# Performance work log

Hardware: AMD Instinct MI355X
Metric: run time of the kernel (lower is better)

## Reference

```python
import jax, jax.numpy as jnp
import numpy as np

NUM_GROUPS = 32
EPS = 1e-5


def group_norm(x, scale, bias):
    # x: [b, c, h, w]
    b, c, h, w = x.shape
    xg = x.reshape(b, NUM_GROUPS, c // NUM_GROUPS, h, w)
    mean = jnp.mean(xg, axis=(2, 3, 4), keepdims=True)
    var = jnp.var(xg, axis=(2, 3, 4), keepdims=True)
    xg = (xg - mean) * jax.lax.rsqrt(var + EPS)
    xn = xg.reshape(b, c, h, w)
    return xn * scale[None, :, None, None] + bias[None, :, None, None]


def conv1x1(x, w, b):
    # x: [b, c_in, h, w], w: [c_out, c_in], b: [c_out]
    return jnp.einsum('bchw,dc->bdhw', x, w) + b[None, :, None, None]


def setup_inputs() -> dict:
    key = jax.random.key(0)
    ks = jax.random.split(key, 11)
    B, C, H, W = 16, 512, 32, 32
    s = 1.0 / np.sqrt(C)
    inp = {
        'x': jax.random.normal(ks[0], (B, C, H, W), jnp.float32),
        'gn_scale': jnp.ones((C,), jnp.float32),
        'gn_bias': jnp.zeros((C,), jnp.float32),
        'wq': jax.random.normal(ks[1], (C, C), jnp.float32) * s,
        'bq': jnp.zeros((C,), jnp.float32),
        'wk': jax.random.normal(ks[2], (C, C), jnp.float32) * s,
        'bk': jnp.zeros((C,), jnp.float32),
        'wv': jax.random.normal(ks[3], (C, C), jnp.float32) * s,
        'bv': jnp.zeros((C,), jnp.float32),
        'wp': jax.random.normal(ks[4], (C, C), jnp.float32) * s,
        'bp': jnp.zeros((C,), jnp.float32),
    }
    return inp


def reference(x, gn_scale, gn_bias, wq, bq, wk, bk, wv, bv, wp, bp):
    b, c, h, w = x.shape
    xn = group_norm(x, gn_scale, gn_bias)
    q = conv1x1(xn, wq, bq).reshape(b, c, h * w)  # [b, c, n]
    k = conv1x1(xn, wk, bk).reshape(b, c, h * w)
    v = conv1x1(xn, wv, bv).reshape(b, c, h * w)
    # attn[b, i, j] = sum_c q[b, c, i] * k[b, c, j]
    attn = jnp.einsum('bci,bcj->bij', q, k) * (c ** -0.5)
    A = jax.nn.softmax(attn, axis=-1)
    # out[b, c, i] = sum_j A[b, i, j] * v[b, c, j]
    out = jnp.einsum('bij,bcj->bci', A, v).reshape(b, c, h, w)
    scores = conv1x1(out, wp, bp)
    return x + scores
```

## Files before the change

### kernel.cpp

```cpp
#include <hip/hip_runtime.h>

typedef __bf16 bf16x8 __attribute__((ext_vector_type(8)));
typedef float  f32x4  __attribute__((ext_vector_type(4)));

__device__ __forceinline__ unsigned short f2bf(float f) {
    union { float f; unsigned int u; } x; x.f = f;
    unsigned int r = (x.u + 0x7FFFu + ((x.u >> 16) & 1u)) >> 16;
    return (unsigned short)r;
}
__device__ __forceinline__ float bf2f(unsigned int hi) {
    union { unsigned int u; float f; } x; x.u = hi; return x.f;
}

typedef const __attribute__((address_space(1))) unsigned short gu16;
typedef __attribute__((address_space(3)))       unsigned short lu16;
__device__ __forceinline__ void gl_lds16(const unsigned short* g, unsigned short* l) {
    __builtin_amdgcn_global_load_lds((gu16*)g, (lu16*)l, 16, 0, 0);
}

__device__ __forceinline__ void stage_tiles(
    const unsigned short* __restrict__ Ab, int lda,
    const unsigned short* __restrict__ Bb, int ldb,
    int k0, unsigned short* Ad, unsigned short* Bd,
    int wave, int r0, int c0)
{
    gl_lds16(Ab + (long)r0 * lda + c0 + k0,        Ad + wave * 512);
    gl_lds16(Ab + (long)(r0 + 64) * lda + c0 + k0, Ad + 2048 + wave * 512);
    gl_lds16(Bb + (long)r0 * ldb + c0 + k0,        Bd + wave * 512);
    gl_lds16(Bb + (long)(r0 + 64) * ldb + c0 + k0, Bd + 2048 + wave * 512);
}

__device__ __forceinline__ void gemm_core_db(
    const unsigned short* __restrict__ Ab, int lda,
    const unsigned short* __restrict__ Bb, int ldb,
    int K, f32x4 (&acc)[4][4],
    unsigned short* As, unsigned short* Bs)
{
    const int tid  = threadIdx.x;
    const int lane = tid & 63;
    const int wave = tid >> 6;
    const int wm   = (wave >> 1) * 64;
    const int wn   = (wave & 1) * 64;
    const int l16  = lane & 15;
    const int quad = lane >> 4;

    const int r0 = wave * 16 + (lane >> 2);
    const int c0 = (lane & 3) * 8;

    stage_tiles(Ab, lda, Bb, ldb, 0, As, Bs, wave, r0, c0);

    int sel = 0;
    for (int k0 = 0; k0 < K; k0 += 32) {
        __syncthreads();
        if (k0 + 32 < K)
            stage_tiles(Ab, lda, Bb, ldb, k0 + 32,
                        As + (sel ^ 1) * 4096, Bs + (sel ^ 1) * 4096, wave, r0, c0);

        const unsigned short* Ap = As + sel * 4096;
        const unsigned short* Bp = Bs + sel * 4096;
        bf16x8 af[4], bfr[4];
        #pragma unroll
        for (int mi = 0; mi < 4; mi++)
            af[mi] = *(const bf16x8*)&Ap[(wm + mi * 16 + l16) * 32 + quad * 8];
        #pragma unroll
        for (int ni = 0; ni < 4; ni++)
            bfr[ni] = *(const bf16x8*)&Bp[(wn + ni * 16 + l16) * 32 + quad * 8];
        #pragma unroll
        for (int mi = 0; mi < 4; mi++)
            #pragma unroll
            for (int ni = 0; ni < 4; ni++)
                acc[mi][ni] = __builtin_amdgcn_mfma_f32_16x16x32_bf16(af[mi], bfr[ni], acc[mi][ni], 0, 0, 0);
        sel ^= 1;
    }
}

template<typename OutT, bool TRANS_OUT, bool HAS_BIAS, bool HAS_RESID,
         bool EXP_SUM, bool ROW_SCALE>
__global__ __launch_bounds__(256) void gemm_k(
    const unsigned short* __restrict__ Ag, long sA, int lda,
    const unsigned short* __restrict__ Bg, long sB, int ldb,
    OutT* __restrict__ Cg, long sC, int ldc,
    const float* __restrict__ bias,
    const float* __restrict__ resid, long sR,
    float* __restrict__ lsum, long sL,
    float alpha, int K)
{
    __shared__ __align__(16) unsigned short As[2 * 4096];
    __shared__ __align__(16) unsigned short Bs[2 * 4096];

    const unsigned short* Ab = Ag + (long)blockIdx.z * sA + (long)(blockIdx.y * 128) * lda;
    const unsigned short* Bb = Bg + (long)blockIdx.z * sB + (long)(blockIdx.x * 128) * ldb;

    f32x4 acc[4][4] = {};
    gemm_core_db(Ab, lda, Bb, ldb, K, acc, As, Bs);

    const int lane = threadIdx.x & 63;
    const int wave = threadIdx.x >> 6;
    const int l16  = lane & 15;
    const int quad = lane >> 4;
    const int mb = blockIdx.y * 128 + (wave >> 1) * 64;
    const int nb = blockIdx.x * 128 + (wave & 1) * 64;

    #pragma unroll
    for (int mi = 0; mi < 4; mi++) {
        float rsum[4];
        if constexpr (EXP_SUM) { rsum[0] = rsum[1] = rsum[2] = rsum[3] = 0.f; }
        #pragma unroll
        for (int ni = 0; ni < 4; ni++) {
            f32x4 v = acc[mi][ni];
            const int m0 = mb + mi * 16 + quad * 4;
            const int n  = nb + ni * 16 + l16;
            float o[4];
            float invl;
            if constexpr (ROW_SCALE) invl = 1.f / lsum[(long)blockIdx.z * sL + n];
            #pragma unroll
            for (int r = 0; r < 4; r++) {
                float val = v[r] * alpha;
                if (HAS_BIAS) val += bias[m0 + r];
                if constexpr (EXP_SUM) { val = __expf(val); rsum[r] += val; }
                if constexpr (ROW_SCALE) val *= invl;
                o[r] = val;
            }
            if constexpr (!TRANS_OUT) {
                const long base = (long)blockIdx.z * sC;
                #pragma unroll
                for (int r = 0; r < 4; r++) {
                    float val = o[r];
                    if (HAS_RESID) val += resid[(long)blockIdx.z * sR + (long)(m0 + r) * ldc + n];
                    long idx = base + (long)(m0 + r) * ldc + n;
                    if constexpr (sizeof(OutT) == 2) ((unsigned short*)Cg)[idx] = f2bf(val);
                    else                              ((float*)Cg)[idx] = val;
                }
            } else {
                const long idx = (long)blockIdx.z * sC + (long)n * ldc + m0;
                if constexpr (sizeof(OutT) == 2) {
                    ushort4 p; p.x = f2bf(o[0]); p.y = f2bf(o[1]); p.z = f2bf(o[2]); p.w = f2bf(o[3]);
                    *(ushort4*)((unsigned short*)Cg + idx) = p;
                } else {
                    float4 p; p.x = o[0]; p.y = o[1]; p.z = o[2]; p.w = o[3];
                    *(float4*)((float*)Cg + idx) = p;
                }
            }
        }
        if constexpr (EXP_SUM) {
            const int m0 = mb + mi * 16 + quad * 4;
            #pragma unroll
            for (int r = 0; r < 4; r++) {
                float s = rsum[r];
                s += __shfl_xor(s, 1); s += __shfl_xor(s, 2);
                s += __shfl_xor(s, 4); s += __shfl_xor(s, 8);
                if (l16 == 0)
                    atomicAdd(&lsum[(long)blockIdx.z * sL + m0 + r], s);
            }
        }
    }
}

__global__ __launch_bounds__(256) void qkv_k(
    const unsigned short* __restrict__ Wqkv,
    const unsigned short* __restrict__ xnT,
    unsigned short* __restrict__ qT,
    unsigned short* __restrict__ kT,
    unsigned short* __restrict__ vB,
    const float* __restrict__ bqkv)
{
    __shared__ __align__(16) unsigned short As[2 * 4096];
    __shared__ __align__(16) unsigned short Bs[2 * 4096];

    const unsigned short* Ab = Wqkv + (long)(blockIdx.y * 128) * 512;
    const unsigned short* Bb = xnT + (long)blockIdx.z * 524288 + (long)(blockIdx.x * 128) * 512;

    f32x4 acc[4][4] = {};
    gemm_core_db(Ab, 512, Bb, 512, 512, acc, As, Bs);

    const int lane = threadIdx.x & 63;
    const int wave = threadIdx.x >> 6;
    const int l16  = lane & 15;
    const int quad = lane >> 4;
    const int mb = blockIdx.y * 128 + (wave >> 1) * 64;
    const int nb = blockIdx.x * 128 + (wave & 1) * 64;

    const int mat = blockIdx.y >> 2;
    const long zb = (long)blockIdx.z * 524288;

    #pragma unroll
    for (int mi = 0; mi < 4; mi++) {
        #pragma unroll
        for (int ni = 0; ni < 4; ni++) {
            f32x4 v = acc[mi][ni];
            const int m0 = mb + mi * 16 + quad * 4;
            const int n  = nb + ni * 16 + l16;
            float o[4];
            #pragma unroll
            for (int r = 0; r < 4; r++) o[r] = v[r] + bqkv[m0 + r];
            const int ml = m0 & 511;
            if (mat == 2) {
                #pragma unroll
                for (int r = 0; r < 4; r++)
                    vB[zb + (long)(ml + r) * 1024 + n] = f2bf(o[r]);
            } else {
                unsigned short* dst = (mat == 0) ? qT : kT;
                ushort4 p; p.x = f2bf(o[0]); p.y = f2bf(o[1]); p.z = f2bf(o[2]); p.w = f2bf(o[3]);
                *(ushort4*)(dst + zb + (long)n * 512 + ml) = p;
            }
        }
    }
}

__global__ __launch_bounds__(256) void gn_k(
    const float* __restrict__ x, const float* __restrict__ gsc,
    const float* __restrict__ gbi, unsigned short* __restrict__ xnT)
{
    __shared__ __align__(16) unsigned short ln[16 * 1024];
    __shared__ float red[8];
    const int b = blockIdx.y, g = blockIdx.x;
    const int tid = threadIdx.x, lane = tid & 63, wv = tid >> 6;

    const float4* x4 = (const float4*)(x + ((long)b * 512 + g * 16) * 1024);
    float4 vals[16];
    float s = 0.f, ss = 0.f;
    #pragma unroll
    for (int i = 0; i < 16; i++) {
        float4 v = x4[tid + i * 256];
        vals[i] = v;
        s  += v.x + v.y + v.z + v.w;
        ss += v.x * v.x + v.y * v.y + v.z * v.z + v.w * v.w;
    }
    for (int o = 32; o; o >>= 1) { s += __shfl_down(s, o); ss += __shfl_down(ss, o); }
    if (lane == 0) { red[wv * 2] = s; red[wv * 2 + 1] = ss; }
    __syncthreads();
    const float S  = red[0] + red[2] + red[4] + red[6];
    const float SS = red[1] + red[3] + red[5] + red[7];
    const float mean = S * (1.f / 16384.f);
    const float var  = SS * (1.f / 16384.f) - mean * mean;
    const float inv  = rsqrtf(var + 1e-5f);

    #pragma unroll
    for (int i = 0; i < 16; i++) {
        const int idx = tid + i * 256;
        const int c   = idx >> 8;
        const float sc = gsc[g * 16 + c] * inv;
        const float bi = gbi[g * 16 + c] - mean * sc;
        float4 v = vals[i];
        ushort4 p;
        p.x = f2bf(v.x * sc + bi); p.y = f2bf(v.y * sc + bi);
        p.z = f2bf(v.z * sc + bi); p.w = f2bf(v.w * sc + bi);
        ((ushort4*)ln)[idx] = p;
    }
    __syncthreads();

    unsigned short* op = xnT + (long)b * 1024 * 512 + g * 16;
    for (int rep = 0; rep < 4; rep++) {
        const int n = rep * 256 + tid;
        union { unsigned short u[16]; uint4 v[2]; } t;
        #pragma unroll
        for (int c = 0; c < 16; c++) t.u[c] = ln[c * 1024 + n];
        *(uint4*)&op[(long)n * 512]     = t.v[0];
        *(uint4*)&op[(long)n * 512 + 8] = t.v[1];
    }
}

__global__ __launch_bounds__(256) void wconv_k(
    const float* __restrict__ w0, const float* __restrict__ w1,
    const float* __restrict__ w2, const float* __restrict__ w3,
    const float* __restrict__ b0, const float* __restrict__ b1,
    const float* __restrict__ b2,
    unsigned short* __restrict__ out, float* __restrict__ bqkv,
    float* __restrict__ lsum)
{
    const int m = blockIdx.y;
    const int i = blockIdx.x * 256 + threadIdx.x;
    if (m == 4) {
        if (i < 384) {
            const int which = i >> 7, off = i & 127;
            const float* src = (which == 0) ? b0 : (which == 1) ? b1 : b2;
            ((float4*)bqkv)[i] = ((const float4*)src)[off];
        }
        if (i < 16384) lsum[i] = 0.f;
        return;
    }
    const float* src = (m == 0) ? w0 : (m == 1) ? w1 : (m == 2) ? w2 : w3;
    float4 v = ((const float4*)src)[i];
    ushort4 o; o.x = f2bf(v.x); o.y = f2bf(v.y); o.z = f2bf(v.z); o.w = f2bf(v.w);
    ((ushort4*)(out + (long)m * 262144))[i] = o;
}

extern "C" void kernel_launch(void* const* d_in, const int* in_sizes, int n_in,
                              void* d_out, int out_size, void* d_ws, size_t ws_size,
                              hipStream_t stream)
{
    const float* x   = (const float*)d_in[0];
    const float* gsc = (const float*)d_in[1];
    const float* gbi = (const float*)d_in[2];
    const float* wq  = (const float*)d_in[3];
    const float* bq  = (const float*)d_in[4];
    const float* wk  = (const float*)d_in[5];
    const float* bk  = (const float*)d_in[6];
    const float* wv  = (const float*)d_in[7];
    const float* bv  = (const float*)d_in[8];
    const float* wp  = (const float*)d_in[9];
    const float* bp  = (const float*)d_in[10];
    float* out = (float*)d_out;

    char* ws = (char*)d_ws;
    unsigned short* xnT = (unsigned short*)(ws);
    unsigned short* qT  = (unsigned short*)(ws + 16777216);
    unsigned short* kT  = (unsigned short*)(ws + 33554432);
    unsigned short* vB  = (unsigned short*)(ws + 50331648);
    unsigned short* Sb  = (unsigned short*)(ws + 67108864);
    unsigned short* Wb  = (unsigned short*)(ws + 100663296);
    float*          bqkv= (float*)        (ws + 102760448);
    float*          Lb  = (float*)        (ws + 102768640);
    unsigned short* OT  = xnT;

    const long sBCN = 512L * 1024;

    wconv_k<<<dim3(256, 5), 256, 0, stream>>>(wq, wk, wv, wp, bq, bk, bv, Wb, bqkv, Lb);
    gn_k<<<dim3(32, 16), 256, 0, stream>>>(x, gsc, gbi, xnT);

    qkv_k<<<dim3(8, 12, 16), 256, 0, stream>>>(Wb, xnT, qT, kT, vB, bqkv);

    gemm_k<unsigned short, false, false, false, true, false>
        <<<dim3(8, 8, 16), 256, 0, stream>>>(
        qT, sBCN, 512, kT, sBCN, 512, Sb, 1048576L, 1024, nullptr, nullptr, 0,
        Lb, 1024, 0.044194173824159216f, 512);

    gemm_k<unsigned short, true, false, false, false, true>
        <<<dim3(8, 4, 16), 256, 0, stream>>>(
        vB, sBCN, 1024, Sb, 1048576L, 1024, OT, sBCN, 512,
        nullptr, nullptr, 0, Lb, 1024, 1.f, 1024);

    gemm_k<float, false, true, true, false, false>
        <<<dim3(8, 4, 16), 256, 0, stream>>>(
        Wb + 786432, 0, 512, OT, sBCN, 512, out, sBCN, 1024, bp, x, sBCN,
        nullptr, 0, 1.f, 512);
}
```

Baseline: 239.4 us.

## Swizzle LDS GEMM tiles and stage bf16 epilogue through LDS for 16-byte stores

Applies an XOR swizzle to the 16-byte column chunks of the A/B tiles, on both the global-to-LDS staging side and the MFMA fragment read side, to reduce LDS bank conflicts. The bf16-output epilogues of the generic GEMM and the QKV kernel now write each wave's 64x64 tile into a swizzled LDS scratch area, then read it back and emit coalesced 16-byte global stores, replacing scattered 2-byte or 8-byte stores. This adds two barriers and some LDS traffic per block and reuses the operand buffers as scratch.

```diff
diff --git a/kernel.cpp b/kernel.cpp
--- a/kernel.cpp
+++ b/kernel.cpp
@@ -7,9 +7,6 @@
     union { float f; unsigned int u; } x; x.f = f;
     unsigned int r = (x.u + 0x7FFFu + ((x.u >> 16) & 1u)) >> 16;
     return (unsigned short)r;
-}
-__device__ __forceinline__ float bf2f(unsigned int hi) {
-    union { unsigned int u; float f; } x; x.u = hi; return x.f;
 }
 
 typedef const __attribute__((address_space(1))) unsigned short gu16;
@@ -45,9 +42,11 @@
     const int quad = lane >> 4;
 
     const int r0 = wave * 16 + (lane >> 2);
-    const int c0 = (lane & 3) * 8;
+    const int c0 = ((lane & 3) ^ ((lane >> 3) & 3)) * 8;
 
     stage_tiles(Ab, lda, Bb, ldb, 0, As, Bs, wave, r0, c0);
+
+    const int sw8 = ((l16 >> 1) & 3) * 8;
 
     int sel = 0;
     for (int k0 = 0; k0 < K; k0 += 32) {
@@ -61,10 +60,10 @@
         bf16x8 af[4], bfr[4];
         #pragma unroll
         for (int mi = 0; mi < 4; mi++)
-            af[mi] = *(const bf16x8*)&Ap[(wm + mi * 16 + l16) * 32 + quad * 8];
+            af[mi] = *(const bf16x8*)&Ap[(wm + mi * 16 + l16) * 32 + ((quad * 8) ^ sw8)];
         #pragma unroll
         for (int ni = 0; ni < 4; ni++)
-            bfr[ni] = *(const bf16x8*)&Bp[(wn + ni * 16 + l16) * 32 + quad * 8];
+            bfr[ni] = *(const bf16x8*)&Bp[(wn + ni * 16 + l16) * 32 + ((quad * 8) ^ sw8)];
         #pragma unroll
         for (int mi = 0; mi < 4; mi++)
             #pragma unroll
@@ -85,8 +84,9 @@
     float* __restrict__ lsum, long sL,
     float alpha, int K)
 {
-    __shared__ __align__(16) unsigned short As[2 * 4096];
-    __shared__ __align__(16) unsigned short Bs[2 * 4096];
+    __shared__ __align__(16) unsigned short LB[16384];
+    unsigned short* As = LB;
+    unsigned short* Bs = LB + 8192;
 
     const unsigned short* Ab = Ag + (long)blockIdx.z * sA + (long)(blockIdx.y * 128) * lda;
     const unsigned short* Bb = Bg + (long)blockIdx.z * sB + (long)(blockIdx.x * 128) * ldb;
@@ -101,56 +101,92 @@
     const int mb = blockIdx.y * 128 + (wave >> 1) * 64;
     const int nb = blockIdx.x * 128 + (wave & 1) * 64;
 
-    #pragma unroll
-    for (int mi = 0; mi < 4; mi++) {
-        float rsum[4];
-        if constexpr (EXP_SUM) { rsum[0] = rsum[1] = rsum[2] = rsum[3] = 0.f; }
-        #pragma unroll
-        for (int ni = 0; ni < 4; ni++) {
-            f32x4 v = acc[mi][ni];
-            const int m0 = mb + mi * 16 + quad * 4;
-            const int n  = nb + ni * 16 + l16;
-            float o[4];
-            float invl;
-            if constexpr (ROW_SCALE) invl = 1.f / lsum[(long)blockIdx.z * sL + n];
-            #pragma unroll
-            for (int r = 0; r < 4; r++) {
-                float val = v[r] * alpha;
-                if (HAS_BIAS) val += bias[m0 + r];
-                if constexpr (EXP_SUM) { val = __expf(val); rsum[r] += val; }
-                if constexpr (ROW_SCALE) val *= invl;
-                o[r] = val;
-            }
-            if constexpr (!TRANS_OUT) {
+    if constexpr (sizeof(OutT) == 2) {
+        __syncthreads();
+        unsigned short* scr = LB + wave * 4096;
+
+        #pragma unroll
+        for (int mi = 0; mi < 4; mi++) {
+            float rsum[4];
+            if constexpr (EXP_SUM) { rsum[0] = rsum[1] = rsum[2] = rsum[3] = 0.f; }
+            #pragma unroll
+            for (int ni = 0; ni < 4; ni++) {
+                f32x4 v = acc[mi][ni];
+                float invl;
+                if constexpr (ROW_SCALE) invl = 1.f / lsum[(long)blockIdx.z * sL + nb + ni * 16 + l16];
+                float o[4];
+                #pragma unroll
+                for (int r = 0; r < 4; r++) {
+                    float val = v[r] * alpha;
+                    if constexpr (HAS_BIAS) val += bias[mb + mi * 16 + quad * 4 + r];
+                    if constexpr (EXP_SUM) { val = __expf(val); rsum[r] += val; }
+                    if constexpr (ROW_SCALE) val *= invl;
+                    o[r] = val;
+                }
+                if constexpr (TRANS_OUT) {
+                    const int nl = ni * 16 + l16;
+                    const int ch = mi * 2 + (quad >> 1);
+                    ushort4 p; p.x = f2bf(o[0]); p.y = f2bf(o[1]); p.z = f2bf(o[2]); p.w = f2bf(o[3]);
+                    *(ushort4*)&scr[nl * 64 + ((ch ^ (nl & 7)) * 8) + (quad & 1) * 4] = p;
+                } else {
+                    #pragma unroll
+                    for (int r = 0; r < 4; r++) {
+                        const int ml = mi * 16 + quad * 4 + r;
+                        const int nc = ni * 2 + (l16 >> 3);
+                        scr[ml * 64 + ((nc ^ (ml & 7)) * 8) + (l16 & 7)] = f2bf(o[r]);
+                    }
+                }
+            }
+            if constexpr (EXP_SUM) {
+                const int m0 = mb + mi * 16 + quad * 4;
+                #pragma unroll
+                for (int r = 0; r < 4; r++) {
+                    float s = rsum[r];
+                    s += __shfl_xor(s, 1); s += __shfl_xor(s, 2);
+                    s += __shfl_xor(s, 4); s += __shfl_xor(s, 8);
+                    if (l16 == 0)
+                        atomicAdd(&lsum[(long)blockIdx.z * sL + m0 + r], s);
+                }
+            }
+        }
+        __syncthreads();
+
+        const int ch2 = lane & 7;
+        const int rr  = lane >> 3;
+        unsigned short* Cs = (unsigned short*)Cg + (long)blockIdx.z * sC;
+        if constexpr (TRANS_OUT) {
+            unsigned short* dst = Cs + mb + ch2 * 8;
+            #pragma unroll
+            for (int it = 0; it < 8; it++) {
+                const int nl = rr + it * 8;
+                uint4 v = *(uint4*)&scr[nl * 64 + ((ch2 ^ (nl & 7)) * 8)];
+                *(uint4*)(dst + (long)(nb + nl) * ldc) = v;
+            }
+        } else {
+            unsigned short* dst = Cs + nb + ch2 * 8;
+            #pragma unroll
+            for (int it = 0; it < 8; it++) {
+                const int ml = rr + it * 8;
+                uint4 v = *(uint4*)&scr[ml * 64 + ((ch2 ^ (ml & 7)) * 8)];
+                *(uint4*)(dst + (long)(mb + ml) * ldc) = v;
+            }
+        }
+    } else {
+        #pragma unroll
+        for (int mi = 0; mi < 4; mi++) {
+            #pragma unroll
+            for (int ni = 0; ni < 4; ni++) {
+                f32x4 v = acc[mi][ni];
+                const int m0 = mb + mi * 16 + quad * 4;
+                const int n  = nb + ni * 16 + l16;
                 const long base = (long)blockIdx.z * sC;
                 #pragma unroll
                 for (int r = 0; r < 4; r++) {
-                    float val = o[r];
+                    float val = v[r] * alpha;
+                    if (HAS_BIAS) val += bias[m0 + r];
                     if (HAS_RESID) val += resid[(long)blockIdx.z * sR + (long)(m0 + r) * ldc + n];
-                    long idx = base + (long)(m0 + r) * ldc + n;
-                    if constexpr (sizeof(OutT) == 2) ((unsigned short*)Cg)[idx] = f2bf(val);
-                    else                              ((float*)Cg)[idx] = val;
+                    ((float*)Cg)[base + (long)(m0 + r) * ldc + n] = val;
                 }
-            } else {
-                const long idx = (long)blockIdx.z * sC + (long)n * ldc + m0;
-                if constexpr (sizeof(OutT) == 2) {
-                    ushort4 p; p.x = f2bf(o[0]); p.y = f2bf(o[1]); p.z = f2bf(o[2]); p.w = f2bf(o[3]);
-                    *(ushort4*)((unsigned short*)Cg + idx) = p;
-                } else {
-                    float4 p; p.x = o[0]; p.y = o[1]; p.z = o[2]; p.w = o[3];
-                    *(float4*)((float*)Cg + idx) = p;
-                }
-            }
-        }
-        if constexpr (EXP_SUM) {
-            const int m0 = mb + mi * 16 + quad * 4;
-            #pragma unroll
-            for (int r = 0; r < 4; r++) {
-                float s = rsum[r];
-                s += __shfl_xor(s, 1); s += __shfl_xor(s, 2);
-                s += __shfl_xor(s, 4); s += __shfl_xor(s, 8);
-                if (l16 == 0)
-                    atomicAdd(&lsum[(long)blockIdx.z * sL + m0 + r], s);
             }
         }
     }
@@ -164,8 +200,9 @@
     unsigned short* __restrict__ vB,
     const float* __restrict__ bqkv)
 {
-    __shared__ __align__(16) unsigned short As[2 * 4096];
-    __shared__ __align__(16) unsigned short Bs[2 * 4096];
+    __shared__ __align__(16) unsigned short LB[16384];
+    unsigned short* As = LB;
+    unsigned short* Bs = LB + 8192;
 
     const unsigned short* Ab = Wqkv + (long)(blockIdx.y * 128) * 512;
     const unsigned short* Bb = xnT + (long)blockIdx.z * 524288 + (long)(blockIdx.x * 128) * 512;
@@ -179,9 +216,11 @@
     const int quad = lane >> 4;
     const int mb = blockIdx.y * 128 + (wave >> 1) * 64;
     const int nb = blockIdx.x * 128 + (wave & 1) * 64;
-
     const int mat = blockIdx.y >> 2;
     const long zb = (long)blockIdx.z * 524288;
+
+    __syncthreads();
+    unsigned short* scr = LB + wave * 4096;
 
     #pragma unroll
     for (int mi = 0; mi < 4; mi++) {
@@ -189,20 +228,44 @@
         for (int ni = 0; ni < 4; ni++) {
             f32x4 v = acc[mi][ni];
             const int m0 = mb + mi * 16 + quad * 4;
-            const int n  = nb + ni * 16 + l16;
             float o[4];
             #pragma unroll
             for (int r = 0; r < 4; r++) o[r] = v[r] + bqkv[m0 + r];
-            const int ml = m0 & 511;
             if (mat == 2) {
                 #pragma unroll
-                for (int r = 0; r < 4; r++)
-                    vB[zb + (long)(ml + r) * 1024 + n] = f2bf(o[r]);
+                for (int r = 0; r < 4; r++) {
+                    const int ml = mi * 16 + quad * 4 + r;
+                    const int nc = ni * 2 + (l16 >> 3);
+                    scr[ml * 64 + ((nc ^ (ml & 7)) * 8) + (l16 & 7)] = f2bf(o[r]);
+                }
             } else {
-                unsigned short* dst = (mat == 0) ? qT : kT;
+                const int nl = ni * 16 + l16;
+                const int ch = mi * 2 + (quad >> 1);
                 ushort4 p; p.x = f2bf(o[0]); p.y = f2bf(o[1]); p.z = f2bf(o[2]); p.w = f2bf(o[3]);
-                *(ushort4*)(dst + zb + (long)n * 512 + ml) = p;
-            }
+                *(ushort4*)&scr[nl * 64 + ((ch ^ (nl & 7)) * 8) + (quad & 1) * 4] = p;
+            }
+        }
+    }
+    __syncthreads();
+
+    const int ch2 = lane & 7;
+    const int rr  = lane >> 3;
+    const int ml0 = mb & 511;
+    if (mat == 2) {
+        unsigned short* dst = vB + zb + nb + ch2 * 8;
+        #pragma unroll
+        for (int it = 0; it < 8; it++) {
+            const int ml = rr + it * 8;
+            uint4 v = *(uint4*)&scr[ml * 64 + ((ch2 ^ (ml & 7)) * 8)];
+            *(uint4*)(dst + (long)(ml0 + ml) * 1024) = v;
+        }
+    } else {
+        unsigned short* dst = ((mat == 0) ? qT : kT) + zb + ml0 + ch2 * 8;
+        #pragma unroll
+        for (int it = 0; it < 8; it++) {
+            const int nl = rr + it * 8;
+            uint4 v = *(uint4*)&scr[nl * 64 + ((ch2 ^ (nl & 7)) * 8)];
+            *(uint4*)(dst + (long)(nb + nl) * 512) = v;
         }
     }
 }
```

Result: faster. 225.9 us (-5.7%).
